# Performance work log

Measured on AMD Instinct MI355X. Metric: run time of the kernel, lower is better.

The kernel has to match this reference:

```python
import jax, jax.numpy as jnp
import numpy as np

B, T, C = 2, 2048, 2048
H, DK, DV, K = 16, 128, 128, 4
KEY_DIM = H * DK
VALUE_DIM = H * DV
CONV_DIM = 2 * KEY_DIM + VALUE_DIM
EPS = 1e-6


def setup_inputs() -> dict:
    key = jax.random.key(0)
    ks = jax.random.split(key, 6)
    s = 0.02
    return {
        "x": jax.random.normal(ks[0], (B, T, C), jnp.float32),
        "input_pos": jnp.arange(T, dtype=jnp.int32),
        "W_qkvz": jax.random.normal(ks[1], (C, CONV_DIM + VALUE_DIM), jnp.float32) * s,
        "W_b": jax.random.normal(ks[2], (C, H), jnp.float32) * s,
        "W_a": jax.random.normal(ks[3], (C, H), jnp.float32) * s,
        "conv_w": jax.random.normal(ks[4], (CONV_DIM, 1, K), jnp.float32) * 0.3,
        "norm_w": jnp.ones((DV,), jnp.float32),
        "W_out": jax.random.normal(ks[5], (VALUE_DIM, C), jnp.float32) * s,
        "conv_state": jnp.zeros((B, CONV_DIM, K), jnp.float32),
        "recurrent_state": jnp.zeros((B, H, DK, DV), jnp.float32),
    }


def _l2norm(a):
    return a / jnp.maximum(jnp.linalg.norm(a, axis=-1, keepdims=True), 1e-12)


def reference(x, input_pos, W_qkvz, W_b, W_a, conv_w, norm_w, W_out,
              conv_state, recurrent_state):
    Bx, Tx, Cx = x.shape
    # reset state when sequence starts at position 0
    keep = 1.0 - (input_pos[0] == 0).astype(x.dtype)
    conv_state = conv_state * keep
    recurrent_state = recurrent_state * keep

    qkvz = x @ W_qkvz                                  # [B,T,conv_dim+value_dim]
    qkv, z = qkvz[..., :CONV_DIM], qkvz[..., CONV_DIM:]
    z = z.reshape(Bx, Tx, H, DV)
    beta = jax.nn.sigmoid(x @ W_b)                     # [B,T,H]
    alpha = jax.nn.sigmoid(x @ W_a)                    # [B,T,H]

    # depthwise causal conv with carried conv_state prefix
    conv_in = jnp.concatenate([conv_state, qkv.transpose(0, 2, 1)], axis=-1)  # [B,conv_dim,K+T]
    y = jax.lax.conv_general_dilated(
        conv_in, conv_w, window_strides=(1,), padding='VALID',
        dimension_numbers=('NCH', 'OIH', 'NCH'), feature_group_count=CONV_DIM)
    y = jax.nn.silu(y[:, :, -Tx:]).transpose(0, 2, 1)  # [B,T,conv_dim]

    q, k, v = jnp.split(y, [KEY_DIM, 2 * KEY_DIM], axis=-1)
    q = _l2norm(q.reshape(Bx, Tx, H, DK))
    k = _l2norm(k.reshape(Bx, Tx, H, DK))
    v = v.reshape(Bx, Tx, H, DV)

    def step(state, xs):
        q_i, k_i, v_i, a_i, b_i = xs                    # [B,H,Dk],[B,H,Dk],[B,H,Dv],[B,H],[B,H]
        new_state = (a_i[..., None, None] * state
                     + b_i[..., None, None] * (k_i[..., :, None] * v_i[..., None, :]))
        out_i = jnp.einsum('bhk,bhkv->bhv', q_i, new_state)
        return new_state, out_i

    xs = (q.transpose(1, 0, 2, 3), k.transpose(1, 0, 2, 3), v.transpose(1, 0, 2, 3),
          alpha.transpose(1, 0, 2), beta.transpose(1, 0, 2))
    _, outs = jax.lax.scan(step, recurrent_state, xs)   # outs: [T,B,H,Dv]
    output = outs.transpose(1, 0, 2, 3)                 # [B,T,H,Dv]

    # RMSNorm over head_v_dim, then gate by sigmoid(z)
    output = output * jax.lax.rsqrt(jnp.mean(output * output, axis=-1, keepdims=True) + EPS) * norm_w
    output = output * jax.nn.sigmoid(z)
    return output.reshape(Bx, Tx, -1) @ W_out
```

## Files before the change

### kernel.cpp

```cpp
#include <hip/hip_runtime.h>
#include <hip/hip_bf16.h>
#include <math.h>

#define Bb 2
#define Tt 2048
#define Cc 2048
#define Hh 16
#define CONVD 6144
#define Mrows 4096
#define NCHUNK 32

typedef __attribute__((ext_vector_type(8))) short short8v;
typedef __attribute__((ext_vector_type(4))) float floatx4;

__device__ __forceinline__ unsigned short f2bf(float f) {
    __hip_bfloat16 h = __float2bfloat16(f);
    return __builtin_bit_cast(unsigned short, h);
}

__device__ __forceinline__ void load_lds16(const void* g, void* l) {
    __builtin_amdgcn_global_load_lds(
        (const __attribute__((address_space(1))) void*)g,
        (__attribute__((address_space(3))) void*)l, 16, 0, 0);
}

__device__ __forceinline__ int swz8(int col) {
    return col ^ (((col >> 5) & 3) << 3);
}

#define LGKM0 asm volatile("s_waitcnt lgkmcnt(0)" ::: "memory")
#define VMC4  asm volatile("s_waitcnt vmcnt(4)" ::: "memory")
#define VMC0  asm volatile("s_waitcnt vmcnt(0)" ::: "memory")
#define SCHB  __builtin_amdgcn_sched_barrier(0)
#define SBAR  __builtin_amdgcn_s_barrier()

__global__ __launch_bounds__(256) void cast_bf16(
    const float* __restrict__ in, unsigned short* __restrict__ out, long n)
{
    long i = ((long)blockIdx.x * 256 + threadIdx.x) * 4;
    if (i + 3 >= n) return;
    float4 f = *(const float4*)(in + i);
    ushort4 o;
    o.x = f2bf(f.x); o.y = f2bf(f.y); o.z = f2bf(f.z); o.w = f2bf(f.w);
    *(ushort4*)(out + i) = o;
}

__global__ __launch_bounds__(256) void transpose_cast(
    const float* __restrict__ W, unsigned short* __restrict__ WT, int Kk, int Nn)
{
    __shared__ float tile[32][33];
    const int n0 = blockIdx.x * 32;
    const int k0 = blockIdx.y * 32;
    const int tx = threadIdx.x & 31;
    const int ty = threadIdx.x >> 5;
#pragma unroll
    for (int r = ty; r < 32; r += 8)
        tile[r][tx] = W[(size_t)(k0 + r) * Nn + n0 + tx];
    __syncthreads();
#pragma unroll
    for (int r = ty; r < 32; r += 8)
        WT[(size_t)(n0 + r) * Kk + k0 + tx] = f2bf(tile[tx][r]);
}

__global__ __launch_bounds__(512) void gemm256(
    const unsigned short* __restrict__ A, const unsigned short* __restrict__ Bt,
    float* __restrict__ C1, float* __restrict__ C2,
    int Kk, int lda, int ldb)
{
    __shared__ __align__(16) unsigned short A_lds[2][256 * 32];
    __shared__ __align__(16) unsigned short B_lds[2][256 * 32];

    const int tid  = threadIdx.x;
    const int wid  = tid >> 6;
    const int lane = tid & 63;
    const int wr = wid >> 2, wc = wid & 3;
    const int l15 = lane & 15, kq = lane >> 4;
    const int rdsw = (kq ^ ((l15 >> 1) & 3)) * 8;
    const int rr = lane >> 2;
    const int ch = (lane & 3) ^ ((lane >> 3) & 3);

    const int nwg = gridDim.x * gridDim.y;
    int bid = blockIdx.y * gridDim.x + blockIdx.x;
    int swz = (bid & 7) * (nwg >> 3) + (bid >> 3);
    const int block_m = (swz / gridDim.x) * 256;
    const int block_n = (swz % gridDim.x) * 256;

    const int NT = Kk >> 5;

#define STAGE256(t) do {                                                     \
    const int kk0 = (t) << 5;                                                \
    unsigned short* la = &A_lds[(t) & 1][0];                                 \
    unsigned short* lb = &B_lds[(t) & 1][0];                                 \
    _Pragma("unroll")                                                        \
    for (int i_ = 0; i_ < 2; ++i_) {                                         \
        const int g_ = wid * 2 + i_;                                         \
        load_lds16(A + (size_t)(block_m + g_ * 16 + rr) * lda + kk0 + ch * 8,\
                   la + g_ * 512);                                           \
        load_lds16(Bt + (size_t)(block_n + g_ * 16 + rr) * ldb + kk0 + ch * 8,\
                   lb + g_ * 512);                                           \
    }                                                                        \
} while (0)

    floatx4 acc[8][4] = {};

    STAGE256(0);
    STAGE256(1);
    VMC4; SCHB; SBAR; SCHB;

    for (int t = 0; t < NT; ++t) {
        const unsigned short* la = &A_lds[t & 1][0];
        const unsigned short* lb = &B_lds[t & 1][0];
        short8v af[8], bf[4];
#pragma unroll
        for (int mf = 0; mf < 8; ++mf)
            af[mf] = *(const short8v*)(la + (wr * 128 + mf * 16 + l15) * 32 + rdsw);
#pragma unroll
        for (int nf = 0; nf < 4; ++nf)
            bf[nf] = *(const short8v*)(lb + (wc * 64 + nf * 16 + l15) * 32 + rdsw);
        LGKM0; SCHB;
        SBAR;
        SCHB;
        if (t + 2 < NT) STAGE256(t + 2);
        SCHB;
        __builtin_amdgcn_s_setprio(1);
#pragma unroll
        for (int mf = 0; mf < 8; ++mf)
#pragma unroll
            for (int nf = 0; nf < 4; ++nf)
                acc[mf][nf] = __builtin_amdgcn_mfma_f32_16x16x32_bf16(
                    af[mf], bf[nf], acc[mf][nf], 0, 0, 0);
        __builtin_amdgcn_s_setprio(0);
        SCHB;
        if (t + 2 < NT)      { VMC4; }
        else if (t + 1 < NT) { VMC0; }
        SCHB; SBAR; SCHB;
    }

    float* Cp; int col0; size_t ldc;
    if (block_n < 6144) { Cp = C1; col0 = block_n;        ldc = 6144; }
    else                { Cp = C2; col0 = block_n - 6144; ldc = 2048; }
#pragma unroll
    for (int mf = 0; mf < 8; ++mf)
#pragma unroll
        for (int nf = 0; nf < 4; ++nf)
#pragma unroll
            for (int r = 0; r < 4; ++r) {
                int row = block_m + wr * 128 + mf * 16 + kq * 4 + r;
                int col = col0 + wc * 64 + nf * 16 + l15;
                Cp[(size_t)row * ldc + col] = acc[mf][nf][r];
            }
#undef STAGE256
}

__global__ __launch_bounds__(256) void gemm_bf16(
    const unsigned short* __restrict__ A, const unsigned short* __restrict__ Bt,
    float* __restrict__ C, int Kk, int lda, int ldb, int ldc)
{
    __shared__ __align__(16) unsigned short A_lds[128 * 64];
    __shared__ __align__(16) unsigned short B_lds[128 * 64];

    const int tid = threadIdx.x;
    const int wv = tid >> 6;
    const int lane = tid & 63;
    const int wr = wv >> 1, wc = wv & 1;
    const int l15 = lane & 15, kq = lane >> 4;
    const int rsw = (l15 & 7) << 3;
    const int block_m = blockIdx.y * 128;
    const int block_n = blockIdx.x * 128;

    const int srow = lane >> 3;
    const int scol = ((lane & 7) ^ srow) << 3;

    floatx4 acc[4][4] = {};

    for (int k0 = 0; k0 < Kk; k0 += 64) {
#pragma unroll
        for (int i = 0; i < 4; ++i) {
            const int lq = wv * 4 + i;
            const unsigned short* asrc =
                A + (size_t)(block_m + lq * 8 + srow) * lda + k0 + scol;
            load_lds16(asrc, &A_lds[lq * 512]);
            const unsigned short* bsrc =
                Bt + (size_t)(block_n + lq * 8 + srow) * ldb + k0 + scol;
            load_lds16(bsrc, &B_lds[lq * 512]);
        }
        __syncthreads();

#pragma unroll
        for (int kk = 0; kk < 2; ++kk) {
            short8v af[4], bf[4];
#pragma unroll
            for (int mf = 0; mf < 4; ++mf) {
                const int row = wr * 64 + mf * 16 + l15;
                af[mf] = *(const short8v*)&A_lds[row * 64 + ((kk * 32 + kq * 8) ^ rsw)];
            }
#pragma unroll
            for (int nf = 0; nf < 4; ++nf) {
                const int row = wc * 64 + nf * 16 + l15;
                bf[nf] = *(const short8v*)&B_lds[row * 64 + ((kk * 32 + kq * 8) ^ rsw)];
            }
#pragma unroll
            for (int mf = 0; mf < 4; ++mf)
#pragma unroll
                for (int nf = 0; nf < 4; ++nf)
                    acc[mf][nf] = __builtin_amdgcn_mfma_f32_16x16x32_bf16(
                        af[mf], bf[nf], acc[mf][nf], 0, 0, 0);
        }
        __syncthreads();
    }

#pragma unroll
    for (int mf = 0; mf < 4; ++mf)
#pragma unroll
        for (int nf = 0; nf < 4; ++nf)
#pragma unroll
            for (int r = 0; r < 4; ++r) {
                int row = block_m + wr * 64 + mf * 16 + kq * 4 + r;
                int col = block_n + wc * 64 + nf * 16 + l15;
                C[(size_t)row * ldc + col] = acc[mf][nf][r];
            }
}

__global__ __launch_bounds__(256) void ab_kernel(
    const float* __restrict__ x, const float* __restrict__ W_b,
    const float* __restrict__ W_a, float* __restrict__ beta,
    float* __restrict__ alpha)
{
    const int row = blockIdx.x;
    const int tid = threadIdx.x;
    float acc[32];
#pragma unroll
    for (int u = 0; u < 32; ++u) acc[u] = 0.f;

    for (int k = tid; k < Cc; k += 256) {
        float xv = x[(size_t)row * Cc + k];
        const float4* wb = (const float4*)(W_b + (size_t)k * 16);
        const float4* wa = (const float4*)(W_a + (size_t)k * 16);
#pragma unroll
        for (int u = 0; u < 4; ++u) {
            float4 b4 = wb[u];
            float4 a4 = wa[u];
            acc[u * 4 + 0] = fmaf(xv, b4.x, acc[u * 4 + 0]);
            acc[u * 4 + 1] = fmaf(xv, b4.y, acc[u * 4 + 1]);
            acc[u * 4 + 2] = fmaf(xv, b4.z, acc[u * 4 + 2]);
            acc[u * 4 + 3] = fmaf(xv, b4.w, acc[u * 4 + 3]);
            acc[16 + u * 4 + 0] = fmaf(xv, a4.x, acc[16 + u * 4 + 0]);
            acc[16 + u * 4 + 1] = fmaf(xv, a4.y, acc[16 + u * 4 + 1]);
            acc[16 + u * 4 + 2] = fmaf(xv, a4.z, acc[16 + u * 4 + 2]);
            acc[16 + u * 4 + 3] = fmaf(xv, a4.w, acc[16 + u * 4 + 3]);
        }
    }
#pragma unroll
    for (int u = 0; u < 32; ++u) {
        float v = acc[u];
        for (int off = 32; off > 0; off >>= 1) v += __shfl_down(v, off);
        acc[u] = v;
    }
    __shared__ float red[4][32];
    const int wv = tid >> 6;
    if ((tid & 63) == 0) {
#pragma unroll
        for (int u = 0; u < 32; ++u) red[wv][u] = acc[u];
    }
    __syncthreads();
    if (tid < 32) {
        float v = red[0][tid] + red[1][tid] + red[2][tid] + red[3][tid];
        float s = 1.f / (1.f + expf(-v));
        if (tid < 16) beta[(size_t)row * 16 + tid] = s;
        else          alpha[(size_t)row * 16 + (tid - 16)] = s;
    }
}

__global__ __launch_bounds__(128) void conv_kernel(
    const float* __restrict__ qkv, const float* __restrict__ conv_w,
    const float* __restrict__ conv_state, const int* __restrict__ input_pos,
    float* __restrict__ qn, float* __restrict__ kn, float* __restrict__ vv)
{
    const int tc = blockIdx.x;
    const int hs = blockIdx.y;
    const int b  = blockIdx.z;
    const int lane = threadIdx.x;
    const int kind = hs >> 4;
    const int h = hs & 15;
    const int c = kind * 2048 + h * 128 + lane;
    const int t0 = tc * 8;
    const float keep = (input_pos[0] == 0) ? 0.f : 1.f;

    const float4 w4 = *(const float4*)(conv_w + (size_t)c * 4);

    float win0, win1, win2;
    {
        float tmp[3];
#pragma unroll
        for (int j = 0; j < 3; ++j) {
            int tau = t0 - 3 + j;
            tmp[j] = (tau >= 0) ? qkv[(size_t)(b * Tt + tau) * CONVD + c]
                   : keep * conv_state[((size_t)b * CONVD + c) * 4 + (tau + 4)];
        }
        win0 = tmp[0]; win1 = tmp[1]; win2 = tmp[2];
    }

    float y[8];
    __shared__ float red[8][2];
#pragma unroll
    for (int i = 0; i < 8; ++i) {
        float xv = qkv[(size_t)(b * Tt + t0 + i) * CONVD + c];
        float a = fmaf(w4.x, win0, fmaf(w4.y, win1, fmaf(w4.z, win2, w4.w * xv)));
        float yy = a / (1.f + expf(-a));
        win0 = win1; win1 = win2; win2 = xv;
        if (kind == 2) {
            vv[(size_t)(b * Tt + t0 + i) * 2048 + h * 128 + lane] = yy;
        } else {
            float sq = yy * yy;
            for (int off = 32; off > 0; off >>= 1) sq += __shfl_down(sq, off);
            if ((lane & 63) == 0) red[i][lane >> 6] = sq;
            y[i] = yy;
        }
    }
    if (kind == 2) return;
    __syncthreads();
#pragma unroll
    for (int i = 0; i < 8; ++i) {
        float tot = red[i][0] + red[i][1];
        float inv = 1.f / fmaxf(sqrtf(tot), 1e-12f);
        float outv = y[i] * inv;
        const size_t oidx = (size_t)(b * Tt + t0 + i) * 2048 + h * 128 + lane;
        if (kind == 0) qn[oidx] = outv;
        else           kn[oidx] = outv;
    }
}

__global__ __launch_bounds__(256) void chunk_prep(
    const float* __restrict__ kn, const float* __restrict__ vv,
    const float* __restrict__ alpha, const float* __restrict__ beta,
    float* __restrict__ logc_g, float* __restrict__ Mbuf)
{
    const int c = blockIdx.x, h = blockIdx.y, b = blockIdx.z;
    const int tid = threadIdx.x;
    const size_t bh = (size_t)b * Hh + h;

    __shared__ float K_lds[32][128];
    __shared__ float V_lds[32][128];
    __shared__ float logc_lds[64];
    __shared__ float b_lds[64];
    __shared__ float wk_lds[64];

    if (tid < 64) {
        const int row = b * Tt + c * 64 + tid;
        float a = alpha[(size_t)row * 16 + h];
        float la = logf(a);
#pragma unroll
        for (int d = 1; d < 64; d <<= 1) {
            float n = __shfl_up(la, d);
            if (tid >= d) la += n;
        }
        logc_lds[tid] = la;
        logc_g[bh * Tt + c * 64 + tid] = la;
        b_lds[tid] = beta[(size_t)row * 16 + h];
    }
    __syncthreads();
    if (tid < 64) {
        wk_lds[tid] = expf(logc_lds[63] - logc_lds[tid]) * b_lds[tid];
    }
    __syncthreads();

    const int ti = tid >> 4;
    const int tj = tid & 15;
    const int tj8sw = swz8(tj * 8);
    float acc[8][8];
#pragma unroll
    for (int i = 0; i < 8; ++i)
#pragma unroll
        for (int j = 0; j < 8; ++j) acc[i][j] = 0.f;

    for (int half = 0; half < 2; ++half) {
        {
            const int sl = tid >> 3;
            const int c0 = (tid & 7) * 16;
            const int grow = b * Tt + c * 64 + half * 32 + sl;
            const float4* kp = (const float4*)(kn + (size_t)grow * 2048 + h * 128 + c0);
            const float4* vp = (const float4*)(vv + (size_t)grow * 2048 + h * 128 + c0);
#pragma unroll
            for (int u = 0; u < 4; ++u) {
                const int cl = c0 + u * 4;
                *(float4*)(&K_lds[sl][cl]) = kp[u];
                *(float4*)(&V_lds[sl][swz8(cl)]) = vp[u];
            }
        }
        __syncthreads();
#pragma unroll 4
        for (int s = 0; s < 32; ++s) {
            float w = wk_lds[half * 32 + s];
            float4 k0 = *(const float4*)(&K_lds[s][ti * 8]);
            float4 k1 = *(const float4*)(&K_lds[s][ti * 8 + 4]);
            float4 v0 = *(const float4*)(&V_lds[s][tj8sw]);
            float4 v1 = *(const float4*)(&V_lds[s][tj8sw + 4]);
            float wk[8] = {w*k0.x, w*k0.y, w*k0.z, w*k0.w, w*k1.x, w*k1.y, w*k1.z, w*k1.w};
            float vf[8] = {v0.x, v0.y, v0.z, v0.w, v1.x, v1.y, v1.z, v1.w};
#pragma unroll
            for (int i = 0; i < 8; ++i)
#pragma unroll
                for (int j = 0; j < 8; ++j)
                    acc[i][j] = fmaf(wk[i], vf[j], acc[i][j]);
        }
        __syncthreads();
    }
    float* mb = Mbuf + ((bh * NCHUNK) + c) * 16384;
#pragma unroll
    for (int i = 0; i < 8; ++i) {
        float4 o0 = {acc[i][0], acc[i][1], acc[i][2], acc[i][3]};
        float4 o1 = {acc[i][4], acc[i][5], acc[i][6], acc[i][7]};
        *(float4*)(mb + (size_t)(ti * 8 + i) * 128 + tj * 8) = o0;
        *(float4*)(mb + (size_t)(ti * 8 + i) * 128 + tj * 8 + 4) = o1;
    }
}

__global__ __launch_bounds__(256) void state_scan(
    float* __restrict__ Mbuf, const float* __restrict__ logc_g,
    const float* __restrict__ rec_state, const int* __restrict__ input_pos)
{
    const size_t g = (size_t)blockIdx.x * 256 + threadIdx.x;
    const int bh = (int)(g >> 14);
    const float keep = (input_pos[0] == 0) ? 0.f : 1.f;

    float S = keep * rec_state[g];
    const float* lc = logc_g + (size_t)bh * Tt;
    float* base = Mbuf + (size_t)(g & ~16383ull) * NCHUNK + (g & 16383);
#pragma unroll 4
    for (int c = 0; c < NCHUNK; ++c) {
        float Atot = expf(lc[c * 64 + 63]);
        float m = base[(size_t)c * 16384];
        base[(size_t)c * 16384] = S;
        S = fmaf(Atot, S, m);
    }
}

__global__ __launch_bounds__(256) void chunk_out(
    const float* __restrict__ qn, const float* __restrict__ kn,
    const float* __restrict__ vv, const float* __restrict__ beta,
    const float* __restrict__ logc_g, const float* __restrict__ Sstates,
    const float* __restrict__ norm_w, const float* __restrict__ zbuf,
    unsigned short* __restrict__ gated_b)
{
    const int c = blockIdx.x, h = blockIdx.y, b = blockIdx.z;
    const int tid = threadIdx.x;
    const int ti = tid >> 4;
    const int tj = tid & 15;
    const size_t bh = (size_t)b * Hh + h;
    const int row0 = b * Tt + c * 64;

    __shared__ float Q_lds[64][132];
    __shared__ float Bf[64 * 68];
    __shared__ float At[64][68];
    __shared__ float logc_s[64], b_s[64];

    {
        const int r = tid >> 2, c0 = (tid & 3) * 32;
        const float4* qp = (const float4*)(qn + (size_t)(row0 + r) * 2048 + h * 128 + c0);
#pragma unroll
        for (int u = 0; u < 8; ++u)
            *(float4*)(&Q_lds[r][c0 + u * 4]) = qp[u];
    }
    if (tid < 64) {
        logc_s[tid] = logc_g[bh * Tt + c * 64 + tid];
        b_s[tid] = beta[(size_t)(row0 + tid) * 16 + h];
    }

    float acc_a[4][4] = {};
    for (int kh = 0; kh < 2; ++kh) {
        __syncthreads();
        {
            const int s = tid >> 2, c0 = (tid & 3) * 16;
            const float* kp = kn + (size_t)(row0 + s) * 2048 + h * 128 + kh * 64 + c0;
#pragma unroll
            for (int u = 0; u < 16; ++u)
                Bf[(c0 + u) * 68 + s] = kp[u];
        }
        __syncthreads();
#pragma unroll 4
        for (int kk = 0; kk < 64; ++kk) {
            float a[4];
#pragma unroll
            for (int r = 0; r < 4; ++r) a[r] = Q_lds[ti * 4 + r][kh * 64 + kk];
            float4 bq = *(const float4*)(&Bf[kk * 68 + tj * 4]);
            float bb[4] = {bq.x, bq.y, bq.z, bq.w};
#pragma unroll
            for (int r = 0; r < 4; ++r)
#pragma unroll
                for (int cc = 0; cc < 4; ++cc)
                    acc_a[r][cc] = fmaf(a[r], bb[cc], acc_a[r][cc]);
        }
    }

#pragma unroll
    for (int r = 0; r < 4; ++r) {
        const int t = ti * 4 + r;
        const float lct = logc_s[t];
#pragma unroll
        for (int cc = 0; cc < 4; ++cc) {
            const int s = tj * 4 + cc;
            float w = (s <= t) ? expf(lct - logc_s[s]) * b_s[s] : 0.f;
            At[t][s] = w * acc_a[r][cc];
        }
    }

    float o[4][8] = {};
    const float* Sbase = Sstates + (bh * NCHUNK + c) * 16384;
    const int tj8sw = swz8(tj * 8);
    for (int kb = 0; kb < 8; ++kb) {
        __syncthreads();
        {
            const int rr = tid >> 4;
            const int cl = (tid & 15) * 8;
            const int sw = swz8(cl);
            const float4* sp = (const float4*)(Sbase + (size_t)(kb * 16 + rr) * 128 + cl);
            *(float4*)(&Bf[rr * 132 + sw]) = sp[0];
            *(float4*)(&Bf[rr * 132 + sw + 4]) = sp[1];
        }
        __syncthreads();
#pragma unroll
        for (int kk = 0; kk < 16; ++kk) {
            float a[4];
#pragma unroll
            for (int r = 0; r < 4; ++r) a[r] = Q_lds[ti * 4 + r][kb * 16 + kk];
            float4 s0 = *(const float4*)(&Bf[kk * 132 + tj8sw]);
            float4 s1 = *(const float4*)(&Bf[kk * 132 + tj8sw + 4]);
            float sv[8] = {s0.x, s0.y, s0.z, s0.w, s1.x, s1.y, s1.z, s1.w};
#pragma unroll
            for (int r = 0; r < 4; ++r)
#pragma unroll
                for (int j = 0; j < 8; ++j)
                    o[r][j] = fmaf(a[r], sv[j], o[r][j]);
        }
    }
#pragma unroll
    for (int r = 0; r < 4; ++r) {
        const float ct = expf(logc_s[ti * 4 + r]);
#pragma unroll
        for (int j = 0; j < 8; ++j) o[r][j] *= ct;
    }

    for (int sh = 0; sh < 2; ++sh) {
        __syncthreads();
        {
            const int rr = tid >> 3;
            const int c0 = (tid & 7) * 16;
            const float4* vp = (const float4*)(vv + (size_t)(row0 + sh * 32 + rr) * 2048 + h * 128 + c0);
#pragma unroll
            for (int u = 0; u < 4; ++u) {
                const int cl = c0 + u * 4;
                *(float4*)(&Bf[rr * 132 + swz8(cl)]) = vp[u];
            }
        }
        __syncthreads();
#pragma unroll 2
        for (int sp = 0; sp < 32; ++sp) {
            const int s = sh * 32 + sp;
            float a[4];
#pragma unroll
            for (int r = 0; r < 4; ++r) a[r] = At[ti * 4 + r][s];
            float4 v0 = *(const float4*)(&Bf[sp * 132 + tj8sw]);
            float4 v1 = *(const float4*)(&Bf[sp * 132 + tj8sw + 4]);
            float vf[8] = {v0.x, v0.y, v0.z, v0.w, v1.x, v1.y, v1.z, v1.w};
#pragma unroll
            for (int r = 0; r < 4; ++r)
#pragma unroll
                for (int j = 0; j < 8; ++j)
                    o[r][j] = fmaf(a[r], vf[j], o[r][j]);
        }
    }

#pragma unroll
    for (int r = 0; r < 4; ++r) {
        float ss = 0.f;
#pragma unroll
        for (int j = 0; j < 8; ++j) ss = fmaf(o[r][j], o[r][j], ss);
        ss += __shfl_xor(ss, 1);
        ss += __shfl_xor(ss, 2);
        ss += __shfl_xor(ss, 4);
        ss += __shfl_xor(ss, 8);
        const float scale = rsqrtf(ss * (1.f / 128.f) + 1e-6f);
        const int t = ti * 4 + r;
        const float* zp = zbuf + (size_t)(row0 + t) * 2048 + h * 128 + tj * 8;
        unsigned short* gp = gated_b + (size_t)(row0 + t) * 2048 + h * 128 + tj * 8;
#pragma unroll
        for (int j = 0; j < 8; ++j) {
            float zv = zp[j];
            float g = o[r][j] * scale * norm_w[tj * 8 + j] * (1.f / (1.f + expf(-zv)));
            gp[j] = f2bf(g);
        }
    }
}

extern "C" void kernel_launch(void* const* d_in, const int* in_sizes, int n_in,
                              void* d_out, int out_size, void* d_ws, size_t ws_size,
                              hipStream_t stream) {
    (void)in_sizes; (void)n_in; (void)out_size; (void)ws_size;
    const float* x          = (const float*)d_in[0];
    const int*   input_pos  = (const int*)d_in[1];
    const float* W_qkvz     = (const float*)d_in[2];
    const float* W_b        = (const float*)d_in[3];
    const float* W_a        = (const float*)d_in[4];
    const float* conv_w     = (const float*)d_in[5];
    const float* norm_w     = (const float*)d_in[6];
    const float* W_out      = (const float*)d_in[7];
    const float* conv_state = (const float*)d_in[8];
    const float* rec_state  = (const float*)d_in[9];
    float* out = (float*)d_out;
    float* ws  = (float*)d_ws;

    float* qkv   = ws;
    float* Mbuf  = ws;
    unsigned short* gated_b = (unsigned short*)(ws + 16777216);
    float* qn    = ws + 25165824ull;
    float* kn    = qn + 8388608ull;
    float* vv    = kn + 8388608ull;
    unsigned short* xb  = (unsigned short*)qn;
    unsigned short* WqT = (unsigned short*)(qn + 4194304ull);
    float* zbuf  = vv + 8388608ull;
    unsigned short* WoT = (unsigned short*)(zbuf + 8388608ull);
    float* alpha = zbuf + 8388608ull + 2097152ull;
    float* beta  = alpha + 65536ull;
    float* logc  = beta + 65536ull;

    cast_bf16<<<8192, 256, 0, stream>>>(x, xb, 8388608L);
    transpose_cast<<<dim3(8192 / 32, 2048 / 32), 256, 0, stream>>>(W_qkvz, WqT, 2048, 8192);
    transpose_cast<<<dim3(2048 / 32, 2048 / 32), 256, 0, stream>>>(W_out, WoT, 2048, 2048);

    gemm256<<<dim3(8192 / 256, Mrows / 256), 512, 0, stream>>>(
        xb, WqT, qkv, zbuf, 2048, 2048, 2048);
    ab_kernel<<<Mrows, 256, 0, stream>>>(x, W_b, W_a, beta, alpha);
    conv_kernel<<<dim3(Tt / 8, 48, Bb), 128, 0, stream>>>(
        qkv, conv_w, conv_state, input_pos, qn, kn, vv);
    chunk_prep<<<dim3(NCHUNK, Hh, Bb), 256, 0, stream>>>(
        kn, vv, alpha, beta, logc, Mbuf);
    state_scan<<<2048, 256, 0, stream>>>(Mbuf, logc, rec_state, input_pos);
    chunk_out<<<dim3(NCHUNK, Hh, Bb), 256, 0, stream>>>(
        qn, kn, vv, beta, logc, Mbuf, norm_w, zbuf, gated_b);
    gemm_bf16<<<dim3(2048 / 128, Mrows / 128), 256, 0, stream>>>(
        gated_b, WoT, out, 2048, 2048, 2048, 2048);
}
```

Baseline: 558.2 us.

## Fuse preprocessing launches, remap GEMM tiles per XCD, widen conv time chunk

Merges the two weight transpose-cast launches into one grid and folds the x-to-bf16 cast into ab_kernel, which now writes xb as it reads x. Both GEMMs get an XCD-aware workgroup remapping so tiles that share operands run on the same die and reuse its L2. The conv kernel now handles 16 timesteps per block instead of 8. Together these cut launch count and redundant passes over x, with a risk of lower occupancy in conv and of strided bf16 stores in ab_kernel.

After: 534.8 us. 1.04x faster.

```diff
diff --git a/kernel.cpp b/kernel.cpp
--- a/kernel.cpp
+++ b/kernel.cpp
@@ -34,20 +34,13 @@
 #define SCHB  __builtin_amdgcn_sched_barrier(0)
 #define SBAR  __builtin_amdgcn_s_barrier()
 
-__global__ __launch_bounds__(256) void cast_bf16(
-    const float* __restrict__ in, unsigned short* __restrict__ out, long n)
-{
-    long i = ((long)blockIdx.x * 256 + threadIdx.x) * 4;
-    if (i + 3 >= n) return;
-    float4 f = *(const float4*)(in + i);
-    ushort4 o;
-    o.x = f2bf(f.x); o.y = f2bf(f.y); o.z = f2bf(f.z); o.w = f2bf(f.w);
-    *(ushort4*)(out + i) = o;
-}
-
-__global__ __launch_bounds__(256) void transpose_cast(
-    const float* __restrict__ W, unsigned short* __restrict__ WT, int Kk, int Nn)
-{
+__global__ __launch_bounds__(256) void transpose_cast2(
+    const float* __restrict__ W1, unsigned short* __restrict__ WT1,
+    const float* __restrict__ W2, unsigned short* __restrict__ WT2)
+{
+    const float* W; unsigned short* WT; int Nn;
+    if (blockIdx.z == 0) { W = W1; WT = WT1; Nn = 8192; }
+    else                 { W = W2; WT = WT2; Nn = 2048; if (blockIdx.x >= 64) return; }
     __shared__ float tile[32][33];
     const int n0 = blockIdx.x * 32;
     const int k0 = blockIdx.y * 32;
@@ -59,7 +52,7 @@
     __syncthreads();
 #pragma unroll
     for (int r = ty; r < 32; r += 8)
-        WT[(size_t)(n0 + r) * Kk + k0 + tx] = f2bf(tile[tx][r]);
+        WT[(size_t)(n0 + r) * 2048 + k0 + tx] = f2bf(tile[tx][r]);
 }
 
 __global__ __launch_bounds__(512) void gemm256(
@@ -79,11 +72,11 @@
     const int rr = lane >> 2;
     const int ch = (lane & 3) ^ ((lane >> 3) & 3);
 
-    const int nwg = gridDim.x * gridDim.y;
-    int bid = blockIdx.y * gridDim.x + blockIdx.x;
-    int swz = (bid & 7) * (nwg >> 3) + (bid >> 3);
-    const int block_m = (swz / gridDim.x) * 256;
-    const int block_n = (swz % gridDim.x) * 256;
+    const int bid = blockIdx.y * 32 + blockIdx.x;
+    const int xcd = bid & 7;
+    const int idx = bid >> 3;
+    const int block_m = ((xcd >> 2) * 8 + (idx >> 3)) * 256;
+    const int block_n = ((xcd & 3) * 8 + (idx & 7)) * 256;
 
     const int NT = Kk >> 5;
 
@@ -165,8 +158,12 @@
     const int wr = wv >> 1, wc = wv & 1;
     const int l15 = lane & 15, kq = lane >> 4;
     const int rsw = (l15 & 7) << 3;
-    const int block_m = blockIdx.y * 128;
-    const int block_n = blockIdx.x * 128;
+
+    const int nwg = gridDim.x * gridDim.y;
+    const int bid = blockIdx.y * gridDim.x + blockIdx.x;
+    const int wgid = (bid & 7) * (nwg >> 3) + (bid >> 3);
+    const int block_m = (wgid / gridDim.x) * 128;
+    const int block_n = (wgid % gridDim.x) * 128;
 
     const int srow = lane >> 3;
     const int scol = ((lane & 7) ^ srow) << 3;
@@ -224,7 +221,7 @@
 __global__ __launch_bounds__(256) void ab_kernel(
     const float* __restrict__ x, const float* __restrict__ W_b,
     const float* __restrict__ W_a, float* __restrict__ beta,
-    float* __restrict__ alpha)
+    float* __restrict__ alpha, unsigned short* __restrict__ xb)
 {
     const int row = blockIdx.x;
     const int tid = threadIdx.x;
@@ -234,6 +231,7 @@
 
     for (int k = tid; k < Cc; k += 256) {
         float xv = x[(size_t)row * Cc + k];
+        xb[(size_t)row * Cc + k] = f2bf(xv);
         const float4* wb = (const float4*)(W_b + (size_t)k * 16);
         const float4* wa = (const float4*)(W_a + (size_t)k * 16);
 #pragma unroll
@@ -283,7 +281,7 @@
     const int kind = hs >> 4;
     const int h = hs & 15;
     const int c = kind * 2048 + h * 128 + lane;
-    const int t0 = tc * 8;
+    const int t0 = tc * 16;
     const float keep = (input_pos[0] == 0) ? 0.f : 1.f;
 
     const float4 w4 = *(const float4*)(conv_w + (size_t)c * 4);
@@ -300,10 +298,10 @@
         win0 = tmp[0]; win1 = tmp[1]; win2 = tmp[2];
     }
 
-    float y[8];
-    __shared__ float red[8][2];
-#pragma unroll
-    for (int i = 0; i < 8; ++i) {
+    float y[16];
+    __shared__ float red[16][2];
+#pragma unroll
+    for (int i = 0; i < 16; ++i) {
         float xv = qkv[(size_t)(b * Tt + t0 + i) * CONVD + c];
         float a = fmaf(w4.x, win0, fmaf(w4.y, win1, fmaf(w4.z, win2, w4.w * xv)));
         float yy = a / (1.f + expf(-a));
@@ -320,7 +318,7 @@
     if (kind == 2) return;
     __syncthreads();
 #pragma unroll
-    for (int i = 0; i < 8; ++i) {
+    for (int i = 0; i < 16; ++i) {
         float tot = red[i][0] + red[i][1];
         float inv = 1.f / fmaxf(sqrtf(tot), 1e-12f);
         float outv = y[i] * inv;
@@ -623,14 +621,12 @@
     float* beta  = alpha + 65536ull;
     float* logc  = beta + 65536ull;
 
-    cast_bf16<<<8192, 256, 0, stream>>>(x, xb, 8388608L);
-    transpose_cast<<<dim3(8192 / 32, 2048 / 32), 256, 0, stream>>>(W_qkvz, WqT, 2048, 8192);
-    transpose_cast<<<dim3(2048 / 32, 2048 / 32), 256, 0, stream>>>(W_out, WoT, 2048, 2048);
+    transpose_cast2<<<dim3(256, 64, 2), 256, 0, stream>>>(W_qkvz, WqT, W_out, WoT);
+    ab_kernel<<<Mrows, 256, 0, stream>>>(x, W_b, W_a, beta, alpha, xb);
 
     gemm256<<<dim3(8192 / 256, Mrows / 256), 512, 0, stream>>>(
         xb, WqT, qkv, zbuf, 2048, 2048, 2048);
-    ab_kernel<<<Mrows, 256, 0, stream>>>(x, W_b, W_a, beta, alpha);
-    conv_kernel<<<dim3(Tt / 8, 48, Bb), 128, 0, stream>>>(
+    conv_kernel<<<dim3(Tt / 16, 48, Bb), 128, 0, stream>>>(
         qkv, conv_w, conv_state, input_pos, qn, kn, vv);
     chunk_prep<<<dim3(NCHUNK, Hh, Bb), 256, 0, stream>>>(
         kn, vv, alpha, beta, logc, Mbuf);
```
